# Kernel optimization log

Hardware: AMD Instinct MI355X
Metric: run time of the kernel (lower is better)

The kernel has to match this reference:

```python
import jax, jax.numpy as jnp
import numpy as np

NUM_HEADS = 16
NUM_GROUPS = 4
NUM_KV_HEADS = NUM_HEADS // NUM_GROUPS  # 4
HEAD_DIM = 64
MAX_DIST = 484


def setup_inputs() -> dict:
    key = jax.random.key(0)
    ks = jax.random.split(key, 8)
    B, S, E, H = 32, 484, 1024, 1024
    kv_dim = HEAD_DIM * NUM_GROUPS  # 256
    s_in = 0.03
    return {
        "query": jax.random.normal(ks[0], (B, S, E), dtype=jnp.float32),
        "key": jax.random.normal(ks[1], (B, S, E), dtype=jnp.float32),
        "value": jax.random.normal(ks[2], (B, S, E), dtype=jnp.float32),
        "Wq": jax.random.normal(ks[3], (E, H), dtype=jnp.float32) * s_in,
        "Wk": jax.random.normal(ks[4], (E, kv_dim), dtype=jnp.float32) * s_in,
        "Wv": jax.random.normal(ks[5], (E, kv_dim), dtype=jnp.float32) * s_in,
        "Wo": jax.random.normal(ks[6], (H, E), dtype=jnp.float32) * s_in,
        "rel_table": jax.random.normal(ks[7], (2 * MAX_DIST - 1, NUM_HEADS), dtype=jnp.float32) * 0.02,
    }


def _rel_bias(rel_table, q_len, k_len):
    # relative position k - q, clipped to [-(MD-1), MD-1], shifted to table index
    rel = jnp.arange(k_len)[None, :] - jnp.arange(q_len)[:, None]
    idx = jnp.clip(rel, -(MAX_DIST - 1), MAX_DIST - 1) + (MAX_DIST - 1)
    bias = rel_table[idx]  # [q, k, heads]
    return jnp.transpose(bias, (2, 0, 1))  # [heads, q, k]


def reference(query, key, value, Wq, Wk, Wv, Wo, rel_table):
    B, Q, _ = query.shape
    K = key.shape[1]
    G, Hkv, D = NUM_GROUPS, NUM_KV_HEADS, HEAD_DIM
    # projections; torch head split: head index = g*Hkv + h
    q = (query @ Wq).reshape(B, Q, G * Hkv, D).transpose(0, 2, 1, 3)
    q = q.reshape(B, G, Hkv, Q, D)  # b g h sq d
    k = (key @ Wk).reshape(B, K, G, D).transpose(0, 2, 1, 3)  # b g sk d
    v = (value @ Wv).reshape(B, K, G, D).transpose(0, 2, 1, 3)  # b g sv d
    scale = jnp.float32(D) ** 0.5
    scores = jnp.einsum('bghqd,bgkd->bghqk', q, k) / scale
    bias = _rel_bias(rel_table, Q, K).reshape(1, G, Hkv, Q, K)
    attn = jax.nn.softmax(scores + bias, axis=-1)
    out = jnp.einsum('bghqk,bgkd->bghqd', attn, v)
    out = out.reshape(B, G * Hkv, Q, D).transpose(0, 2, 1, 3).reshape(B, Q, G * Hkv * D)
    return out @ Wo
```

## Files before the change

### kernel.cpp

```cpp
#include <hip/hip_runtime.h>
#include <hip/hip_bf16.h>

typedef __attribute__((ext_vector_type(8))) short short8;
typedef __attribute__((ext_vector_type(4))) float f32x4;
typedef __attribute__((ext_vector_type(4))) unsigned uintx4;

#define B_  32
#define S_  484
#define E_  1024
#define NH  16
#define SP  512
#define M_  (B_*S_)

static __device__ __forceinline__ ushort f2bf(float f) {
  union { float f; unsigned u; } v; v.f = f;
  unsigned u = v.u;
  return (ushort)((u + 0x7FFFu + ((u >> 16) & 1u)) >> 16);
}

static __device__ __forceinline__ unsigned cvt_pk_bf16(float lo, float hi) {
  unsigned r;
  asm("v_cvt_pk_bf16_f32 %0, %1, %2" : "=v"(r) : "v"(lo), "v"(hi));
  return r;
}

#define GLOAD_LDS16(gp, lp) \
  __builtin_amdgcn_global_load_lds((const __attribute__((address_space(1))) void*)(gp), \
                                   (__attribute__((address_space(3))) void*)(lp), 16, 0, 0)

__global__ __launch_bounds__(256)
void cvt_f32_bf16(const float* __restrict__ x, ushort* __restrict__ y, int n4) {
  int i = blockIdx.x * 256 + threadIdx.x;
  int stride = gridDim.x * 256;
  for (; i < n4; i += stride) {
    float4 v = ((const float4*)x)[i];
    ushort4 h;
    h.x = f2bf(v.x); h.y = f2bf(v.y); h.z = f2bf(v.z); h.w = f2bf(v.w);
    ((ushort4*)y)[i] = h;
  }
}

__global__ __launch_bounds__(256)
void transpose_convert(const float* __restrict__ W, ushort* __restrict__ WT, int K, int N) {
  __shared__ float tile[32][33];
  int k0 = blockIdx.y * 32, n0 = blockIdx.x * 32;
  int tx = threadIdx.x, ty = threadIdx.y;
  for (int i = ty; i < 32; i += 8) tile[i][tx] = W[(size_t)(k0 + i) * N + n0 + tx];
  __syncthreads();
  for (int i = ty; i < 32; i += 8) WT[(size_t)(n0 + i) * K + k0 + tx] = f2bf(tile[tx][i]);
}

template<int EPI, int NXLOG>
__global__ __launch_bounds__(256)
void gemm_cnt(const ushort* __restrict__ A, const ushort* __restrict__ BT,
              void* __restrict__ Cout, int N, int K, float oscale) {
  __shared__ alignas(16) ushort sA[3][128 * 32];
  __shared__ alignas(16) ushort sB[3][128 * 32];
  const int tid = threadIdx.x;
  const int lane = tid & 63, w = tid >> 6;

  const int nwg = gridDim.x;
  const int qq = nwg >> 3, rr = nwg & 7;
  const int x = blockIdx.x & 7, seq = blockIdx.x >> 3;
  const int logical = x * qq + (x < rr ? x : rr) + seq;
  const int m0 = (logical >> NXLOG) * 128;
  const int n0 = (logical & ((1 << NXLOG) - 1)) * 128;
  const int NK = K >> 5;

  const int srow = w * 32 + (lane >> 2);
  const int scol = (lane & 3) * 8;
  const ushort* gA0 = A  + (size_t)(m0 + srow) * K + scol;
  const ushort* gB0 = BT + (size_t)(n0 + srow) * K + scol;

  const int wr = w >> 1, wc = w & 1;
  const int g4 = lane >> 4, l16 = lane & 15;
  const int aoff = (wr * 64 + l16) * 32 + 8 * g4;
  const int boff = (wc * 64 + l16) * 32 + 8 * g4;

  f32x4 acc[4][4] = {};

  auto stage = [&](int kt, int buf) {
    const ushort* ga = gA0 + kt * 32;
    const ushort* gb = gB0 + kt * 32;
    GLOAD_LDS16(ga,          &sA[buf][(w * 32) * 32]);
    GLOAD_LDS16(ga + 16 * K, &sA[buf][(w * 32 + 16) * 32]);
    GLOAD_LDS16(gb,          &sB[buf][(w * 32) * 32]);
    GLOAD_LDS16(gb + 16 * K, &sB[buf][(w * 32 + 16) * 32]);
  };

  stage(0, 0);
  stage(1, 1);

  int cur = 0;
  for (int kt = 0; kt < NK; ++kt) {
    if (kt + 1 < NK) asm volatile("s_waitcnt vmcnt(4)" ::: "memory");
    else             asm volatile("s_waitcnt vmcnt(0)" ::: "memory");
    asm volatile("s_waitcnt lgkmcnt(0)" ::: "memory");
    __builtin_amdgcn_s_barrier();
    if (kt + 2 < NK) {
      int nb = cur + 2; if (nb >= 3) nb -= 3;
      stage(kt + 2, nb);
    }
    const ushort* pa = &sA[cur][aoff];
    const ushort* pb = &sB[cur][boff];
    short8 af[4], bf[4];
#pragma unroll
    for (int i = 0; i < 4; ++i) {
      af[i] = *(const short8*)(pa + i * 16 * 32);
      bf[i] = *(const short8*)(pb + i * 16 * 32);
    }
#pragma unroll
    for (int mi = 0; mi < 4; ++mi)
#pragma unroll
      for (int ni = 0; ni < 4; ++ni)
        acc[mi][ni] = __builtin_amdgcn_mfma_f32_16x16x32_bf16(af[mi], bf[ni], acc[mi][ni], 0, 0, 0);
    if (++cur >= 3) cur = 0;
  }

#pragma unroll
  for (int mi = 0; mi < 4; ++mi) {
#pragma unroll
    for (int ni = 0; ni < 4; ++ni) {
#pragma unroll
      for (int r = 0; r < 4; ++r) {
        int m = m0 + wr * 64 + mi * 16 + g4 * 4 + r;
        int n = n0 + wc * 64 + ni * 16 + l16;
        float vv = acc[mi][ni][r];
        if (EPI == 2) {
          ((float*)Cout)[(size_t)m * N + n] = vv;
        } else {
          int b = m / S_, pos = m % S_;
          ushort hv = f2bf(vv * oscale);
          ((ushort*)Cout)[(((size_t)b * NH + (n >> 6)) * SP + pos) * 64 + (n & 63)] = hv;
        }
      }
    }
  }
}

template<int EPI, int SWZ, int NXLOG>
__global__ __launch_bounds__(256)
void gemm_bt(const float* __restrict__ Ain, const ushort* __restrict__ BT,
             void* __restrict__ Cout, int N, int K, int HN, float oscale) {
  __shared__ alignas(16) ushort sA[2][128 * 32];
  __shared__ alignas(16) ushort sB[2][128 * 32];
  const int tid = threadIdx.x;
  const int lane = tid & 63, w = tid >> 6;

  const int nwg = gridDim.x;
  const int qq = nwg >> 3, rr = nwg & 7;
  const int x = blockIdx.x & 7, seq = blockIdx.x >> 3;
  const int logical = x * qq + (x < rr ? x : rr) + seq;
  const int m0 = (logical >> NXLOG) * 128;
  const int n0 = (logical & ((1 << NXLOG) - 1)) * 128;
  const int NK = K >> 5;

  const int srow = w * 32 + (lane >> 2);
  const int scol = (lane & 3) * 8;
  const ushort* gB0 = BT + (size_t)(n0 + srow) * K + scol;

  const int arow = w * 32 + (lane >> 1);
  const int acol = (lane & 1) * 16;
  const float* gA0f = Ain + (size_t)(m0 + arow) * K + acol;

  const int wr = w >> 1, wc = w & 1;
  const int g4 = lane >> 4, l16 = lane & 15;
  const int aoff = (wr * 64 + l16) * 32 + 8 * g4;
  const int boff = (wc * 64 + l16) * 32 + 8 * g4;

  f32x4 acc[4][4] = {};
  float4 fA0, fA1, fA2, fA3;

  auto issueA = [&](int kt) {
    const float4* p = (const float4*)(gA0f + kt * 32);
    fA0 = p[0]; fA1 = p[1]; fA2 = p[2]; fA3 = p[3];
  };
  auto writeA = [&](int buf) {
    unsigned d0 = cvt_pk_bf16(fA0.x, fA0.y), d1 = cvt_pk_bf16(fA0.z, fA0.w);
    unsigned d2 = cvt_pk_bf16(fA1.x, fA1.y), d3 = cvt_pk_bf16(fA1.z, fA1.w);
    unsigned d4 = cvt_pk_bf16(fA2.x, fA2.y), d5 = cvt_pk_bf16(fA2.z, fA2.w);
    unsigned d6 = cvt_pk_bf16(fA3.x, fA3.y), d7 = cvt_pk_bf16(fA3.z, fA3.w);
    ushort* dst = &sA[buf][arow * 32 + acol];
    uintx4 q0 = {d0, d1, d2, d3}, q1 = {d4, d5, d6, d7};
    *(uintx4*)dst = q0;
    *(uintx4*)(dst + 8) = q1;
  };

  issueA(0);
  GLOAD_LDS16(gB0,          &sB[0][(w * 32) * 32]);
  GLOAD_LDS16(gB0 + 16 * K, &sB[0][(w * 32 + 16) * 32]);
  writeA(0);

  for (int kt = 0; kt < NK; ++kt) {
    __syncthreads();
    const int nb = (kt + 1) & 1;
    if (kt + 1 < NK) {
      const ushort* gb = gB0 + (kt + 1) * 32;
      GLOAD_LDS16(gb,          &sB[nb][(w * 32) * 32]);
      GLOAD_LDS16(gb + 16 * K, &sB[nb][(w * 32 + 16) * 32]);
      issueA(kt + 1);
    }
    const ushort* pa = &sA[kt & 1][aoff];
    const ushort* pb = &sB[kt & 1][boff];
    short8 af[4], bf[4];
#pragma unroll
    for (int i = 0; i < 4; ++i) {
      af[i] = *(const short8*)(pa + i * 16 * 32);
      bf[i] = *(const short8*)(pb + i * 16 * 32);
    }
#pragma unroll
    for (int mi = 0; mi < 4; ++mi)
#pragma unroll
      for (int ni = 0; ni < 4; ++ni)
        acc[mi][ni] = __builtin_amdgcn_mfma_f32_16x16x32_bf16(af[mi], bf[ni], acc[mi][ni], 0, 0, 0);
    if (kt + 1 < NK) writeA(nb);
  }

#pragma unroll
  for (int mi = 0; mi < 4; ++mi) {
#pragma unroll
    for (int ni = 0; ni < 4; ++ni) {
#pragma unroll
      for (int r = 0; r < 4; ++r) {
        int m = m0 + wr * 64 + mi * 16 + g4 * 4 + r;
        int n = n0 + wc * 64 + ni * 16 + l16;
        float vv = acc[mi][ni][r];
        int b = m / S_, pos = m % S_;
        if (EPI == 0) {
          int dd = n & 63;
          if (SWZ) dd ^= (pos & 7) << 3;
          ushort hv = f2bf(vv * oscale);
          ((ushort*)Cout)[(((size_t)b * HN + (n >> 6)) * SP + pos) * 64 + dd] = hv;
        } else {
          int local = pos & 31;
          int j = (local < 16) ? (2 * local) : (2 * local - 31);
          int pf_ = (pos & ~31) | (j ^ ((n & 3) << 3));
          ushort hv = f2bf(vv);
          ((ushort*)Cout)[(((size_t)b * HN + (n >> 6)) * 64 + (n & 63)) * SP + pf_] = hv;
        }
      }
    }
  }
}

__global__ __launch_bounds__(256)
void attn_kernel(const ushort* __restrict__ qp, const ushort* __restrict__ kp,
                 const ushort* __restrict__ vpT, const float* __restrict__ rel,
                 ushort* __restrict__ ao) {
  __shared__ float sBias[1056];
  __shared__ alignas(16) ushort sK[2][32 * 64];
  __shared__ alignas(16) ushort sV[2][64 * 32];
  __shared__ alignas(16) ushort sP[4][16 * 40];
  const int tid = threadIdx.x;
  const int blk = blockIdx.x;
  const int logical = (blk & 7) * 512 + (blk >> 3);
  const int qt = logical & 7, head = (logical >> 3) & 15, b = logical >> 7;
  const int g = head >> 2;
  const float LOG2E = 1.44269504f;
  for (int t = tid; t < 1056; t += 256)
    sBias[t] = (t >= 32 && t < 999) ? rel[(t - 32) * 16 + head] * LOG2E : -1e30f;

  const int lane = tid & 63, w = tid >> 6;
  const int g4 = lane >> 4, l16 = lane & 15;
  const int qw = qt * 64 + w * 16;

  const ushort* qbase = qp + (((size_t)b * NH + head) * SP + qw + l16) * 64;
  short8 qf0 = *(const short8*)(qbase + 8 * g4);
  short8 qf1 = *(const short8*)(qbase + 32 + 8 * g4);

  const ushort* kSrc = kp  + ((size_t)b * 4 + g) * SP * 64 + (tid >> 3) * 64 + (tid & 7) * 8;
  const ushort* vSrc = vpT + ((size_t)b * 4 + g) * 64 * SP + (tid >> 2) * SP + (tid & 3) * 8;

  f32x4 acc[4] = {};
  float ps[4] = {0.f, 0.f, 0.f, 0.f};
  const int ib = l16 - (qw + g4 * 4) + 483 + 32;
  ushort* sPw = &sP[w][0];

  const int kswz  = (l16 & 7) << 3;
  const int kOff0 = l16 * 64 + ((8 * g4) ^ kswz);
  const int kOff1 = l16 * 64 + ((32 + 8 * g4) ^ kswz);
  const int vOff  = l16 * 32 + 8 * (g4 ^ (l16 & 3));

  GLOAD_LDS16(kSrc, &sK[0][w * 512]);
  GLOAD_LDS16(vSrc, &sV[0][w * 512]);

  for (int kt = 0; kt < 16; ++kt) {
    __syncthreads();
    if (kt + 1 < 16) {
      GLOAD_LDS16(kSrc + (kt + 1) * 2048, &sK[(kt + 1) & 1][w * 512]);
      GLOAD_LDS16(vSrc + (kt + 1) * 32,   &sV[(kt + 1) & 1][w * 512]);
    }
    const ushort* sk = &sK[kt & 1][0];
    const ushort* sv = &sV[kt & 1][0];
    short8 kf0 = *(const short8*)(sk + kOff0);
    short8 kf1 = *(const short8*)(sk + kOff1);
    short8 kf2 = *(const short8*)(sk + 1024 + kOff0);
    short8 kf3 = *(const short8*)(sk + 1024 + kOff1);
    f32x4 s0 = {}, s1 = {};
    s0 = __builtin_amdgcn_mfma_f32_16x16x32_bf16(qf0, kf0, s0, 0, 0, 0);
    s0 = __builtin_amdgcn_mfma_f32_16x16x32_bf16(qf1, kf1, s0, 0, 0, 0);
    s1 = __builtin_amdgcn_mfma_f32_16x16x32_bf16(qf0, kf2, s1, 0, 0, 0);
    s1 = __builtin_amdgcn_mfma_f32_16x16x32_bf16(qf1, kf3, s1, 0, 0, 0);

    const int k0 = kt * 32;
#pragma unroll
    for (int r = 0; r < 4; ++r) {
      int i0 = ib + k0 - r;
      float p0 = __builtin_amdgcn_exp2f(s0[r] + sBias[i0]);
      float p1 = __builtin_amdgcn_exp2f(s1[r] + sBias[i0 + 16]);
      if (kt == 15) {
        p0 = (k0 + l16 < S_) ? p0 : 0.f;
        p1 = (k0 + 16 + l16 < S_) ? p1 : 0.f;
      }
      ps[r] += p0 + p1;
      *(unsigned*)(sPw + (g4 * 4 + r) * 40 + 2 * l16) = cvt_pk_bf16(p0, p1);
    }
    short8 pf = *(const short8*)(sPw + l16 * 40 + 8 * g4);
#pragma unroll
    for (int nt = 0; nt < 4; ++nt) {
      short8 vf = *(const short8*)(sv + vOff + nt * 512);
      acc[nt] = __builtin_amdgcn_mfma_f32_16x16x32_bf16(pf, vf, acc[nt], 0, 0, 0);
    }
  }

#pragma unroll
  for (int off = 1; off < 16; off <<= 1) {
#pragma unroll
    for (int r = 0; r < 4; ++r) ps[r] += __shfl_xor(ps[r], off, 64);
  }

#pragma unroll
  for (int r = 0; r < 4; ++r) {
    int q_abs = qw + g4 * 4 + r;
    if (q_abs < S_) {
      float inv = 1.f / ps[r];
#pragma unroll
      for (int nt = 0; nt < 4; ++nt) {
        int dd = nt * 16 + l16;
        ao[((size_t)b * S_ + q_abs) * 1024 + head * 64 + dd] = f2bf(acc[nt][r] * inv);
      }
    }
  }
}

extern "C" void kernel_launch(void* const* d_in, const int* in_sizes, int n_in,
                              void* d_out, int out_size, void* d_ws, size_t ws_size,
                              hipStream_t stream) {
  const float* query = (const float*)d_in[0];
  const float* key   = (const float*)d_in[1];
  const float* value = (const float*)d_in[2];
  const float* Wq    = (const float*)d_in[3];
  const float* Wk    = (const float*)d_in[4];
  const float* Wv    = (const float*)d_in[5];
  const float* Wo    = (const float*)d_in[6];
  const float* rel   = (const float*)d_in[7];

  char* ws = (char*)d_ws;
  size_t off = 0;
  auto alloc = [&](size_t bytes) { char* p = ws + off; off += (bytes + 255) & ~(size_t)255; return p; };

  const size_t MEelems = (size_t)M_ * E_;
  ushort* qb  = (ushort*)alloc(MEelems * 2);
  ushort* wqT = (ushort*)alloc((size_t)1024 * 1024 * 2);
  ushort* wkT = (ushort*)alloc((size_t)256 * 1024 * 2);
  ushort* wvT = (ushort*)alloc((size_t)256 * 1024 * 2);
  ushort* woT = (ushort*)alloc((size_t)1024 * 1024 * 2);
  ushort* qp  = (ushort*)alloc((size_t)B_ * NH * SP * 64 * 2);
  ushort* kp  = (ushort*)alloc((size_t)B_ * 4 * SP * 64 * 2);
  ushort* vp  = (ushort*)alloc((size_t)B_ * 4 * 64 * SP * 2);
  ushort* ao  = (ushort*)alloc(MEelems * 2);

  cvt_f32_bf16<<<2048, 256, 0, stream>>>(query, qb, (int)(MEelems / 4));

  transpose_convert<<<dim3(32, 32), dim3(32, 8), 0, stream>>>(Wq, wqT, 1024, 1024);
  transpose_convert<<<dim3(8, 32),  dim3(32, 8), 0, stream>>>(Wk, wkT, 1024, 256);
  transpose_convert<<<dim3(8, 32),  dim3(32, 8), 0, stream>>>(Wv, wvT, 1024, 256);
  transpose_convert<<<dim3(32, 32), dim3(32, 8), 0, stream>>>(Wo, woT, 1024, 1024);

  const float QSCALE = 0.125f * 1.44269504f;
  gemm_cnt<0,3><<<968, 256, 0, stream>>>(qb, wqT, qp, 1024, 1024, QSCALE);
  gemm_bt<0,1,1><<<242, 256, 0, stream>>>(key,   wkT, kp, 256, 1024, 4, 1.0f);
  gemm_bt<1,1,1><<<242, 256, 0, stream>>>(value, wvT, vp, 256, 1024, 4, 1.0f);

  attn_kernel<<<4096, 256, 0, stream>>>(qp, kp, vp, rel, ao);

  gemm_cnt<2,3><<<968, 256, 0, stream>>>(ao, woT, d_out, 1024, 1024, 1.0f);
}
```

Before: 297.4 us.

## Use 256x256 tiles with 512-thread blocks for Q and output projection GEMMs

Replaces the 128x128-tile, 256-thread bf16 GEMM with a 256x256-tile, 512-thread version for the Q projection and output projection. Each wave now computes a 128x64 sub-tile with 32 accumulators, raising arithmetic intensity per LDS load and cutting global traffic per output. Rows past M are clamped on load and masked on store. The trade-off is more LDS (96KB), more registers per thread, and only 244 workgroups, which is fewer than two waves of blocks across the CUs and may cause tail imbalance.

```diff
diff --git a/kernel.cpp b/kernel.cpp
--- a/kernel.cpp
+++ b/kernel.cpp
@@ -50,12 +50,13 @@
   for (int i = ty; i < 32; i += 8) WT[(size_t)(n0 + i) * K + k0 + tx] = f2bf(tile[tx][i]);
 }
 
-template<int EPI, int NXLOG>
-__global__ __launch_bounds__(256)
-void gemm_cnt(const ushort* __restrict__ A, const ushort* __restrict__ BT,
-              void* __restrict__ Cout, int N, int K, float oscale) {
-  __shared__ alignas(16) ushort sA[3][128 * 32];
-  __shared__ alignas(16) ushort sB[3][128 * 32];
+template<int EPI>
+__global__ __launch_bounds__(512)
+void gemm_cnt256(const ushort* __restrict__ A, const ushort* __restrict__ BT,
+                 void* __restrict__ Cout, float oscale) {
+  const int K = 1024, N = 1024, NK = 32;
+  __shared__ alignas(16) ushort sA[3][256 * 32];
+  __shared__ alignas(16) ushort sB[3][256 * 32];
   const int tid = threadIdx.x;
   const int lane = tid & 63, w = tid >> 6;
 
@@ -63,29 +64,27 @@
   const int qq = nwg >> 3, rr = nwg & 7;
   const int x = blockIdx.x & 7, seq = blockIdx.x >> 3;
   const int logical = x * qq + (x < rr ? x : rr) + seq;
-  const int m0 = (logical >> NXLOG) * 128;
-  const int n0 = (logical & ((1 << NXLOG) - 1)) * 128;
-  const int NK = K >> 5;
-
-  const int srow = w * 32 + (lane >> 2);
-  const int scol = (lane & 3) * 8;
-  const ushort* gA0 = A  + (size_t)(m0 + srow) * K + scol;
-  const ushort* gB0 = BT + (size_t)(n0 + srow) * K + scol;
-
-  const int wr = w >> 1, wc = w & 1;
+  const int m0 = (logical >> 2) * 256;
+  const int n0 = (logical & 3) * 256;
+
+  const int brow = tid >> 2, bcol = (tid & 3) * 8;
+  const int rowA0 = min(m0 + brow, M_ - 1);
+  const int rowA1 = min(m0 + brow + 128, M_ - 1);
+  const ushort* gA0 = A + (size_t)rowA0 * K + bcol;
+  const ushort* gA1 = A + (size_t)rowA1 * K + bcol;
+  const ushort* gB0 = BT + (size_t)(n0 + brow) * K + bcol;
+  const int dst = tid * 8;
+
+  const int wr = w >> 2, wc = w & 3;
   const int g4 = lane >> 4, l16 = lane & 15;
-  const int aoff = (wr * 64 + l16) * 32 + 8 * g4;
-  const int boff = (wc * 64 + l16) * 32 + 8 * g4;
-
-  f32x4 acc[4][4] = {};
+
+  f32x4 acc[8][4] = {};
 
   auto stage = [&](int kt, int buf) {
-    const ushort* ga = gA0 + kt * 32;
-    const ushort* gb = gB0 + kt * 32;
-    GLOAD_LDS16(ga,          &sA[buf][(w * 32) * 32]);
-    GLOAD_LDS16(ga + 16 * K, &sA[buf][(w * 32 + 16) * 32]);
-    GLOAD_LDS16(gb,          &sB[buf][(w * 32) * 32]);
-    GLOAD_LDS16(gb + 16 * K, &sB[buf][(w * 32 + 16) * 32]);
+    GLOAD_LDS16(gA0 + kt * 32,           &sA[buf][dst]);
+    GLOAD_LDS16(gA1 + kt * 32,           &sA[buf][dst + 4096]);
+    GLOAD_LDS16(gB0 + kt * 32,           &sB[buf][dst]);
+    GLOAD_LDS16(gB0 + kt * 32 + 128 * K, &sB[buf][dst + 4096]);
   };
 
   stage(0, 0);
@@ -101,16 +100,15 @@
       int nb = cur + 2; if (nb >= 3) nb -= 3;
       stage(kt + 2, nb);
     }
-    const ushort* pa = &sA[cur][aoff];
-    const ushort* pb = &sB[cur][boff];
-    short8 af[4], bf[4];
-#pragma unroll
-    for (int i = 0; i < 4; ++i) {
-      af[i] = *(const short8*)(pa + i * 16 * 32);
-      bf[i] = *(const short8*)(pb + i * 16 * 32);
-    }
-#pragma unroll
-    for (int mi = 0; mi < 4; ++mi)
+    const ushort* pa = &sA[cur][(wr * 128 + l16) * 32 + 8 * g4];
+    const ushort* pb = &sB[cur][(wc * 64 + l16) * 32 + 8 * g4];
+    short8 af[8], bf[4];
+#pragma unroll
+    for (int i = 0; i < 8; ++i) af[i] = *(const short8*)(pa + i * 16 * 32);
+#pragma unroll
+    for (int i = 0; i < 4; ++i) bf[i] = *(const short8*)(pb + i * 16 * 32);
+#pragma unroll
+    for (int mi = 0; mi < 8; ++mi)
 #pragma unroll
       for (int ni = 0; ni < 4; ++ni)
         acc[mi][ni] = __builtin_amdgcn_mfma_f32_16x16x32_bf16(af[mi], bf[ni], acc[mi][ni], 0, 0, 0);
@@ -118,20 +116,22 @@
   }
 
 #pragma unroll
-  for (int mi = 0; mi < 4; ++mi) {
+  for (int mi = 0; mi < 8; ++mi) {
 #pragma unroll
     for (int ni = 0; ni < 4; ++ni) {
 #pragma unroll
       for (int r = 0; r < 4; ++r) {
-        int m = m0 + wr * 64 + mi * 16 + g4 * 4 + r;
+        int m = m0 + wr * 128 + mi * 16 + g4 * 4 + r;
         int n = n0 + wc * 64 + ni * 16 + l16;
-        float vv = acc[mi][ni][r];
-        if (EPI == 2) {
-          ((float*)Cout)[(size_t)m * N + n] = vv;
-        } else {
-          int b = m / S_, pos = m % S_;
-          ushort hv = f2bf(vv * oscale);
-          ((ushort*)Cout)[(((size_t)b * NH + (n >> 6)) * SP + pos) * 64 + (n & 63)] = hv;
+        if (m < M_) {
+          float vv = acc[mi][ni][r];
+          if (EPI == 2) {
+            ((float*)Cout)[(size_t)m * N + n] = vv;
+          } else {
+            int b = m / S_, pos = m % S_;
+            ushort hv = f2bf(vv * oscale);
+            ((ushort*)Cout)[(((size_t)b * NH + (n >> 6)) * SP + pos) * 64 + (n & 63)] = hv;
+          }
         }
       }
     }
@@ -180,10 +180,10 @@
     unsigned d2 = cvt_pk_bf16(fA1.x, fA1.y), d3 = cvt_pk_bf16(fA1.z, fA1.w);
     unsigned d4 = cvt_pk_bf16(fA2.x, fA2.y), d5 = cvt_pk_bf16(fA2.z, fA2.w);
     unsigned d6 = cvt_pk_bf16(fA3.x, fA3.y), d7 = cvt_pk_bf16(fA3.z, fA3.w);
-    ushort* dst = &sA[buf][arow * 32 + acol];
+    ushort* dstp = &sA[buf][arow * 32 + acol];
     uintx4 q0 = {d0, d1, d2, d3}, q1 = {d4, d5, d6, d7};
-    *(uintx4*)dst = q0;
-    *(uintx4*)(dst + 8) = q1;
+    *(uintx4*)dstp = q0;
+    *(uintx4*)(dstp + 8) = q1;
   };
 
   issueA(0);
@@ -378,11 +378,11 @@
   transpose_convert<<<dim3(32, 32), dim3(32, 8), 0, stream>>>(Wo, woT, 1024, 1024);
 
   const float QSCALE = 0.125f * 1.44269504f;
-  gemm_cnt<0,3><<<968, 256, 0, stream>>>(qb, wqT, qp, 1024, 1024, QSCALE);
+  gemm_cnt256<0><<<244, 512, 0, stream>>>(qb, wqT, qp, QSCALE);
   gemm_bt<0,1,1><<<242, 256, 0, stream>>>(key,   wkT, kp, 256, 1024, 4, 1.0f);
   gemm_bt<1,1,1><<<242, 256, 0, stream>>>(value, wvT, vp, 256, 1024, 4, 1.0f);
 
   attn_kernel<<<4096, 256, 0, stream>>>(qp, kp, vp, rel, ao);
 
-  gemm_cnt<2,3><<<968, 256, 0, stream>>>(ao, woT, d_out, 1024, 1024, 1.0f);
-}
+  gemm_cnt256<2><<<244, 512, 0, stream>>>(ao, woT, d_out, 1.0f);
+}
```

Result: no change. 298.5 us (+0.4%).
